# Performance work log

Measured on AMD Instinct MI355X. Metric: run time of the kernel, lower is better.

## Reference

```python
import jax, jax.numpy as jnp
import numpy as np
from jax import lax

HEADS, DHEAD, LMARK, PINV_ITERS = 8, 64, 256, 6
LN_EPS = 1e-5
DIM_IN, DIM_HID, N_CLASSES, N_INST = 1024, 512, 2, 16384


def layer_norm(x, g, b):
    mu = x.mean(-1, keepdims=True)
    var = ((x - mu) ** 2).mean(-1, keepdims=True)
    return (x - mu) * lax.rsqrt(var + LN_EPS) * g + b


def pinv_iter(x):
    # Newton-Schulz Moore-Penrose iteration (lucidrains nystrom-attention)
    ax = jnp.abs(x)
    z = jnp.swapaxes(x, -1, -2) / (ax.sum(-1).max() * ax.sum(-2).max())
    I = jnp.eye(x.shape[-1], dtype=x.dtype)
    for _ in range(PINV_ITERS):
        xz = x @ z
        z = 0.25 * z @ (13.0 * I - xz @ (15.0 * I - xz @ (7.0 * I - xz)))
    return z


def nystrom_attention(x, qkv_w, out_w, out_b, res_w):
    b, n, _ = x.shape
    pad = (-n) % LMARK  # pad at FRONT so n divisible by num_landmarks
    xp = jnp.pad(x, ((0, 0), (pad, 0), (0, 0)))
    npad = n + pad
    qkv = xp @ qkv_w.T  # (b, npad, 3*h*d)
    q, k, v = jnp.split(qkv, 3, axis=-1)
    sh = lambda t: t.reshape(b, npad, HEADS, DHEAD).transpose(0, 2, 1, 3)  # bhnd
    q, k, v = sh(q), sh(k), sh(v)
    q = q * (DHEAD ** -0.5)
    l = npad // LMARK  # tokens per landmark
    lm = lambda t: t.reshape(b, HEADS, LMARK, l, DHEAD).mean(3)
    ql, kl = lm(q), lm(k)
    a1 = jax.nn.softmax(jnp.einsum('bhid,bhjd->bhij', q, kl), -1)   # (b,h,npad,m)
    a2 = jax.nn.softmax(jnp.einsum('bhid,bhjd->bhij', ql, kl), -1)  # (b,h,m,m)
    a3 = jax.nn.softmax(jnp.einsum('bhid,bhjd->bhij', ql, k), -1)   # (b,h,m,npad)
    out = (a1 @ pinv_iter(a2)) @ (a3 @ v)
    # depthwise residual conv over sequence dim per head: kernel (33,1)
    res = lax.conv_general_dilated(v, res_w, (1, 1), [(16, 16), (0, 0)],
                                   dimension_numbers=('NCHW', 'OIHW', 'NCHW'),
                                   feature_group_count=HEADS)
    out = out + res
    out = out.transpose(0, 2, 1, 3).reshape(b, npad, HEADS * DHEAD)
    out = out @ out_w.T + out_b
    return out[:, -n:]


def depthwise(x, w, b, k):
    y = lax.conv_general_dilated(x, w, (1, 1), [(k // 2, k // 2)] * 2,
                                 dimension_numbers=('NCHW', 'OIHW', 'NCHW'),
                                 feature_group_count=x.shape[1])
    return y + b[None, :, None, None]


def ppeg(x, w7, b7, w5, b5, w3, b3):
    B, n1, C = x.shape
    cls_t, feat = x[:, :1], x[:, 1:]
    H = int(round(float(np.sqrt(n1 - 1))))
    f = feat.transpose(0, 2, 1).reshape(B, C, H, H)
    f = f + depthwise(f, w7, b7, 7) + depthwise(f, w5, b5, 5) + depthwise(f, w3, b3, 3)
    f = f.reshape(B, C, H * H).transpose(0, 2, 1)
    return jnp.concatenate([cls_t, f], axis=1)


def setup_inputs() -> dict:
    key = jax.random.key(0)
    ks = jax.random.split(key, 32)
    s = 0.02
    inner = HEADS * DHEAD
    d = {
        'X': jax.random.normal(ks[0], (1, N_INST, DIM_IN), jnp.float32),
        'fc1_w': jax.random.normal(ks[1], (DIM_HID, DIM_IN)) * s,
        'fc1_b': jnp.zeros((DIM_HID,)),
        'cls_token': jax.random.normal(ks[2], (1, 1, DIM_HID)),
        'ln1_g': jnp.ones((DIM_HID,)), 'ln1_b': jnp.zeros((DIM_HID,)),
        'qkv1_w': jax.random.normal(ks[3], (3 * inner, DIM_HID)) * s,
        'out1_w': jax.random.normal(ks[4], (DIM_HID, inner)) * s,
        'out1_b': jnp.zeros((DIM_HID,)),
        'res1_w': jax.random.normal(ks[5], (HEADS, 1, 33, 1)) * s,
        'w7': jax.random.normal(ks[6], (DIM_HID, 1, 7, 7)) * s, 'b7': jnp.zeros((DIM_HID,)),
        'w5': jax.random.normal(ks[7], (DIM_HID, 1, 5, 5)) * s, 'b5': jnp.zeros((DIM_HID,)),
        'w3': jax.random.normal(ks[8], (DIM_HID, 1, 3, 3)) * s, 'b3': jnp.zeros((DIM_HID,)),
        'ln2_g': jnp.ones((DIM_HID,)), 'ln2_b': jnp.zeros((DIM_HID,)),
        'qkv2_w': jax.random.normal(ks[9], (3 * inner, DIM_HID)) * s,
        'out2_w': jax.random.normal(ks[10], (DIM_HID, inner)) * s,
        'out2_b': jnp.zeros((DIM_HID,)),
        'res2_w': jax.random.normal(ks[11], (HEADS, 1, 33, 1)) * s,
        'lnf_g': jnp.ones((DIM_HID,)), 'lnf_b': jnp.zeros((DIM_HID,)),
        'fc2_w': jax.random.normal(ks[12], (N_CLASSES, DIM_HID)) * s,
        'fc2_b': jnp.zeros((N_CLASSES,)),
    }
    return d


def reference(X, fc1_w, fc1_b, cls_token, ln1_g, ln1_b, qkv1_w, out1_w, out1_b, res1_w,
              w7, b7, w5, b5, w3, b3, ln2_g, ln2_b, qkv2_w, out2_w, out2_b, res2_w,
              lnf_g, lnf_b, fc2_w, fc2_b):
    h = jax.nn.relu(X @ fc1_w.T + fc1_b)  # (1, N, dim_hid)
    B, Hn, C = h.shape
    _H = int(np.ceil(np.sqrt(Hn)))
    add_len = _H * _H - Hn
    h = jnp.concatenate([h, h[:, :add_len]], axis=1)  # pad to square by cycling
    h = jnp.concatenate([jnp.broadcast_to(cls_token, (B, 1, C)), h], axis=1)
    h = h + nystrom_attention(layer_norm(h, ln1_g, ln1_b), qkv1_w, out1_w, out1_b, res1_w)
    h = ppeg(h, w7, b7, w5, b5, w3, b3)
    h = h + nystrom_attention(layer_norm(h, ln2_g, ln2_b), qkv2_w, out2_w, out2_b, res2_w)
    h = layer_norm(h, lnf_g, lnf_b)[:, 0]
    return h @ fc2_w.T + fc2_b  # (1, n_classes)
```

## Files before the change

kernel.cpp:

```cpp
#include <hip/hip_runtime.h>
#include <hip/hip_bf16.h>

static const int S    = 16640;
static const int PADR = 255;
static const int NT   = 16385;
static const int CH   = 512;

typedef unsigned short u16;
typedef __attribute__((ext_vector_type(8))) short short8_t;
typedef __attribute__((ext_vector_type(4))) float float4_t;

__device__ __forceinline__ float b2f(u16 x) {
  union { unsigned u; float f; } t; t.u = (unsigned)x << 16; return t.f;
}
__device__ __forceinline__ u16 f2b(float x) {
  union { float f; unsigned u; } t; t.f = x;
  unsigned r = t.u + 0x7fff + ((t.u >> 16) & 1);
  return (u16)(r >> 16);
}

__device__ __forceinline__ float warpSum(float v) {
#pragma unroll
  for (int off = 32; off; off >>= 1) v += __shfl_xor(v, off);
  return v;
}
__device__ __forceinline__ float warpMax(float v) {
#pragma unroll
  for (int off = 32; off; off >>= 1) v = fmaxf(v, __shfl_xor(v, off));
  return v;
}
__device__ __forceinline__ float blockSum(float v) {
  __shared__ float sm[8];
  int lane = threadIdx.x & 63, wv = threadIdx.x >> 6;
  v = warpSum(v);
  __syncthreads();
  if (lane == 0) sm[wv] = v;
  __syncthreads();
  float t = 0.f;
  int nw = blockDim.x >> 6;
  for (int i = 0; i < nw; i++) t += sm[i];
  return t;
}
__device__ __forceinline__ float blockMax(float v) {
  __shared__ float sm[8];
  int lane = threadIdx.x & 63, wv = threadIdx.x >> 6;
  v = warpMax(v);
  __syncthreads();
  if (lane == 0) sm[wv] = v;
  __syncthreads();
  float t = -1e30f;
  int nw = blockDim.x >> 6;
  for (int i = 0; i < nw; i++) t = fmaxf(t, sm[i]);
  return t;
}

__global__ __launch_bounds__(256) void cvt_f2b(const float* __restrict__ in,
                                               u16* __restrict__ out, long n) {
  long i = ((long)blockIdx.x * 256 + threadIdx.x) * 4;
  if (i + 3 < n) {
    float4 v = *(const float4*)(in + i);
    out[i] = f2b(v.x); out[i + 1] = f2b(v.y); out[i + 2] = f2b(v.z); out[i + 3] = f2b(v.w);
  } else {
    for (long j = i; j < n; j++) out[j] = f2b(in[j]);
  }
}

__global__ __launch_bounds__(256) void wm_transpose(const float* __restrict__ Wm,
                                                    u16* __restrict__ WmT) {
  int n = blockIdx.x, head = blockIdx.y, k = threadIdx.x;
  WmT[((long)head * 64 + n) * 256 + k] = f2b(Wm[(long)head * 16384 + k * 64 + n]);
}

template <typename TA, int EPI>
__global__ __launch_bounds__(256) void mfma_gemm(
    const TA* __restrict__ A, const u16* __restrict__ B, float* __restrict__ C,
    const float* __restrict__ bias, int M, int N, int K,
    int lda, int ldb, int ldc,
    float alpha, float beta,
    u16* __restrict__ q_o, u16* __restrict__ k_o, u16* __restrict__ v_o, long s64)
{
  __shared__ u16 As[128][40];
  __shared__ u16 Bs[128][40];
  const int tid = threadIdx.x;
  const int m0 = blockIdx.y * 128, n0 = blockIdx.x * 128;
  const int wid = tid >> 6, lane = tid & 63;
  const int wr = wid >> 1, wc = wid & 1;
  const int l15 = lane & 15, l16 = lane >> 4;
  const int arow = tid >> 1, aseg = (tid & 1) * 16;
  float4_t acc[4][4] = {};

  for (int k0 = 0; k0 < K; k0 += 32) {
    {
      int gm = m0 + arow;
      u16 tmp[16];
      if (gm < M) {
        const TA* src = A + (long)gm * lda + k0 + aseg;
        if constexpr (sizeof(TA) == 2) {
          *(short8_t*)&tmp[0] = *(const short8_t*)src;
          *(short8_t*)&tmp[8] = *(const short8_t*)(src + 8);
        } else {
#pragma unroll
          for (int i4 = 0; i4 < 4; i4++) {
            float4 f = *(const float4*)((const float*)src + i4 * 4);
            tmp[i4 * 4 + 0] = f2b(f.x); tmp[i4 * 4 + 1] = f2b(f.y);
            tmp[i4 * 4 + 2] = f2b(f.z); tmp[i4 * 4 + 3] = f2b(f.w);
          }
        }
      } else {
#pragma unroll
        for (int i = 0; i < 16; i++) tmp[i] = 0;
      }
      *(short8_t*)&As[arow][aseg]     = *(short8_t*)&tmp[0];
      *(short8_t*)&As[arow][aseg + 8] = *(short8_t*)&tmp[8];
    }
    {
      int gn = n0 + arow;
      short8_t v0 = {}, v1 = {};
      if (gn < N) {
        const u16* src = B + (long)gn * ldb + k0 + aseg;
        v0 = *(const short8_t*)src; v1 = *(const short8_t*)(src + 8);
      }
      *(short8_t*)&Bs[arow][aseg]     = v0;
      *(short8_t*)&Bs[arow][aseg + 8] = v1;
    }
    __syncthreads();
    short8_t af[4], bfr[4];
#pragma unroll
    for (int i = 0; i < 4; i++)
      af[i] = *(const short8_t*)&As[wr * 64 + i * 16 + l15][l16 * 8];
#pragma unroll
    for (int i = 0; i < 4; i++)
      bfr[i] = *(const short8_t*)&Bs[wc * 64 + i * 16 + l15][l16 * 8];
#pragma unroll
    for (int i = 0; i < 4; i++)
#pragma unroll
      for (int j = 0; j < 4; j++)
        acc[i][j] = __builtin_amdgcn_mfma_f32_16x16x32_bf16(af[i], bfr[j], acc[i][j], 0, 0, 0);
    __syncthreads();
  }

#pragma unroll
  for (int mi = 0; mi < 4; mi++) {
#pragma unroll
    for (int ni = 0; ni < 4; ni++) {
#pragma unroll
      for (int j = 0; j < 4; j++) {
        int r = m0 + wr * 64 + mi * 16 + l16 * 4 + j;
        int c = n0 + wc * 64 + ni * 16 + l15;
        if (r >= M || c >= N) continue;
        float v = acc[mi][ni][j];
        if constexpr (EPI == 0) {
          long idx = (long)r * ldc + c;
          float o = alpha * v;
          if (bias) o += bias[c];
          if (beta != 0.f) o += beta * C[idx];
          C[idx] = o;
        } else if constexpr (EPI == 1) {
          long idx = (long)r * ldc + c;
          C[idx] = fmaxf(v + bias[c], 0.f);
        } else {
          int sec = c >> 9, hcol = c & 511;
          int head = hcol >> 6, d = hcol & 63;
          u16* dst = (sec == 0) ? q_o : (sec == 1 ? k_o : v_o);
          float o = (sec == 0) ? v * alpha : v;
          dst[(long)head * s64 + (long)r * 64 + d] = f2b(o);
        }
      }
    }
  }
}

template <int MODE>
__global__ __launch_bounds__(256) void pinv_gemm(
    const float* __restrict__ A, const float* __restrict__ B,
    float* __restrict__ C, float* __restrict__ C2, float alpha, float beta)
{
  __shared__ u16 Ah[32][40], Al[32][40], Bh[32][40], Bl[32][40];
  const int tid = threadIdx.x;
  const long zoff = (long)blockIdx.z << 16;
  A += zoff; B += zoff; C += zoff;
  if constexpr (MODE == 3) C2 += zoff;
  const int m0 = blockIdx.y * 32, n0 = blockIdx.x * 32;
  const int wid = tid >> 6, lane = tid & 63;
  const int wr = wid >> 1, wc = wid & 1;
  const int l15 = lane & 15, l16 = lane >> 4;
  const int arow = tid >> 3, acol = (tid & 7) * 4;
  float4_t acc = {};

  for (int k0 = 0; k0 < 256; k0 += 32) {
    {
      float4 va = *(const float4*)(A + (long)(m0 + arow) * 256 + k0 + acol);
      float4 vb = *(const float4*)(B + (long)(k0 + arow) * 256 + n0 + acol);
      float fa[4] = {va.x, va.y, va.z, va.w};
      float fb[4] = {vb.x, vb.y, vb.z, vb.w};
#pragma unroll
      for (int i = 0; i < 4; i++) {
        u16 hi = f2b(fa[i]);
        Ah[arow][acol + i] = hi;
        Al[arow][acol + i] = f2b(fa[i] - b2f(hi));
        u16 hj = f2b(fb[i]);
        Bh[acol + i][arow] = hj;
        Bl[acol + i][arow] = f2b(fb[i] - b2f(hj));
      }
    }
    __syncthreads();
    short8_t ah = *(const short8_t*)&Ah[wr * 16 + l15][l16 * 8];
    short8_t al = *(const short8_t*)&Al[wr * 16 + l15][l16 * 8];
    short8_t bh = *(const short8_t*)&Bh[wc * 16 + l15][l16 * 8];
    short8_t bl = *(const short8_t*)&Bl[wc * 16 + l15][l16 * 8];
    acc = __builtin_amdgcn_mfma_f32_16x16x32_bf16(ah, bh, acc, 0, 0, 0);
    acc = __builtin_amdgcn_mfma_f32_16x16x32_bf16(ah, bl, acc, 0, 0, 0);
    acc = __builtin_amdgcn_mfma_f32_16x16x32_bf16(al, bh, acc, 0, 0, 0);
    __syncthreads();
  }

#pragma unroll
  for (int j = 0; j < 4; j++) {
    int r = m0 + wr * 16 + l16 * 4 + j;
    int c = n0 + wc * 16 + l15;
    long idx = (long)r * 256 + c;
    float v = acc[j];
    if constexpr (MODE == 0) {
      C[idx] = alpha * v;
    } else if constexpr (MODE == 3) {
      C[idx] = v;
      C2[idx] = ((r == c) ? beta : 0.f) - v;
    } else {
      C[idx] = ((r == c) ? beta : 0.f) - v;
    }
  }
}

__global__ __launch_bounds__(256) void attn_a1(
    const u16* __restrict__ qb, const u16* __restrict__ klb,
    const u16* __restrict__ WmT, float* __restrict__ F, long s64)
{
  __shared__ u16 KW[256 * 72];
  __shared__ u16 Ps[64 * 136];
  const int tid = threadIdx.x;
  const int w = tid >> 6, lane = tid & 63;
  const int l15 = lane & 15, l16 = lane >> 4;
  const int head = blockIdx.y;
  const int row0 = blockIdx.x * 64 + w * 16;

  const u16* klh = klb + (long)head * 16384;
#pragma unroll
  for (int i = 0; i < 4; i++) {
    int idx = tid + i * 256;
    int row = idx >> 2, seg = (idx & 3) << 4;
    const u16* src = klh + row * 64 + seg;
    *(short8_t*)&KW[row * 72 + seg]     = *(const short8_t*)src;
    *(short8_t*)&KW[row * 72 + seg + 8] = *(const short8_t*)(src + 8);
  }
  short8_t aq[2];
#pragma unroll
  for (int slab = 0; slab < 2; slab++)
    aq[slab] = *(const short8_t*)(qb + (long)head * s64 + (long)(row0 + l15) * 64 + slab * 32 + l16 * 8);
  __syncthreads();

  float4_t sacc[16] = {};
#pragma unroll
  for (int nt = 0; nt < 16; nt++)
#pragma unroll
    for (int slab = 0; slab < 2; slab++) {
      short8_t bfr = *(const short8_t*)&KW[(nt * 16 + l15) * 72 + slab * 32 + l16 * 8];
      sacc[nt] = __builtin_amdgcn_mfma_f32_16x16x32_bf16(aq[slab], bfr, sacc[nt], 0, 0, 0);
    }
  float rcp[4];
#pragma unroll
  for (int reg = 0; reg < 4; reg++) {
    float m = -1e30f;
#pragma unroll
    for (int nt = 0; nt < 16; nt++) m = fmaxf(m, sacc[nt][reg]);
#pragma unroll
    for (int mk = 1; mk <= 8; mk <<= 1) m = fmaxf(m, __shfl_xor(m, mk));
    float s = 0.f;
#pragma unroll
    for (int nt = 0; nt < 16; nt++) { float e = __expf(sacc[nt][reg] - m); sacc[nt][reg] = e; s += e; }
#pragma unroll
    for (int mk = 1; mk <= 8; mk <<= 1) s += __shfl_xor(s, mk);
    rcp[reg] = 1.f / s;
  }
  __syncthreads();

  const u16* wmh = WmT + (long)head * 16384;
#pragma unroll
  for (int i = 0; i < 4; i++) {
    int idx = tid + i * 256;
    int row = idx >> 4, seg = (idx & 15) << 4;
    const u16* src = wmh + row * 256 + seg;
    *(short8_t*)&KW[row * 264 + seg]     = *(const short8_t*)src;
    *(short8_t*)&KW[row * 264 + seg + 8] = *(const short8_t*)(src + 8);
  }
#pragma unroll
  for (int nt = 0; nt < 8; nt++)
#pragma unroll
    for (int reg = 0; reg < 4; reg++)
      Ps[(w * 16 + 4 * l16 + reg) * 136 + nt * 16 + l15] = f2b(sacc[nt][reg]);
  __syncthreads();

  float4_t oacc[4] = {};
#pragma unroll
  for (int ks = 0; ks < 4; ks++) {
    short8_t pa = *(const short8_t*)&Ps[(w * 16 + l15) * 136 + ks * 32 + l16 * 8];
#pragma unroll
    for (int vt = 0; vt < 4; vt++) {
      short8_t bv = *(const short8_t*)&KW[(vt * 16 + l15) * 264 + ks * 32 + l16 * 8];
      oacc[vt] = __builtin_amdgcn_mfma_f32_16x16x32_bf16(pa, bv, oacc[vt], 0, 0, 0);
    }
  }
#pragma unroll
  for (int nt = 8; nt < 16; nt++)
#pragma unroll
    for (int reg = 0; reg < 4; reg++)
      Ps[(w * 16 + 4 * l16 + reg) * 136 + (nt - 8) * 16 + l15] = f2b(sacc[nt][reg]);
#pragma unroll
  for (int ks = 4; ks < 8; ks++) {
    short8_t pa = *(const short8_t*)&Ps[(w * 16 + l15) * 136 + (ks - 4) * 32 + l16 * 8];
#pragma unroll
    for (int vt = 0; vt < 4; vt++) {
      short8_t bv = *(const short8_t*)&KW[(vt * 16 + l15) * 264 + ks * 32 + l16 * 8];
      oacc[vt] = __builtin_amdgcn_mfma_f32_16x16x32_bf16(pa, bv, oacc[vt], 0, 0, 0);
    }
  }
#pragma unroll
  for (int vt = 0; vt < 4; vt++)
#pragma unroll
    for (int reg = 0; reg < 4; reg++) {
      int r = row0 + 4 * l16 + reg;
      F[(long)r * CH + head * 64 + vt * 16 + l15] = oacc[vt][reg] * rcp[reg];
    }
}

__global__ __launch_bounds__(256) void attn_a3v_split(
    const u16* __restrict__ qlb, const u16* __restrict__ kb,
    const u16* __restrict__ vb,
    float* __restrict__ pm, float* __restrict__ pl, float* __restrict__ poacc,
    long s64)
{
  __shared__ u16 Vt[64][136];
  __shared__ u16 Kt[128 * 72];
  __shared__ u16 Ps[4][16][136];
  const int tid = threadIdx.x;
  const int w = tid >> 6, lane = tid & 63;
  const int l15 = lane & 15, l16 = lane >> 4;
  const int head = blockIdx.y;
  const int split = blockIdx.z;
  const int row0 = blockIdx.x * 64 + w * 16;

  short8_t aq[2];
#pragma unroll
  for (int slab = 0; slab < 2; slab++)
    aq[slab] = *(const short8_t*)(qlb + (long)head * 16384 + (long)(row0 + l15) * 64 + slab * 32 + l16 * 8);

  float m[4], l[4];
  float4_t oacc[4] = {};
#pragma unroll
  for (int r = 0; r < 4; r++) { m[r] = -1e30f; l[r] = 0.f; }

  const u16* kh = kb + (long)head * s64;
  const u16* vh = vb + (long)head * s64;
  const int vrow = tid >> 1, vhalf = (tid & 1) * 32;

  const int kt0 = split * 10;
  for (int kt = kt0; kt < kt0 + 10; kt++) {
    const int j0 = kt * 128;
    __syncthreads();
    {
      const u16* src = vh + (long)(j0 + vrow) * 64 + vhalf;
#pragma unroll
      for (int i = 0; i < 32; i++) Vt[vhalf + i][vrow] = src[i];
    }
#pragma unroll
    for (int i = 0; i < 2; i++) {
      int idx = tid + i * 256;
      int row = idx >> 2, seg = (idx & 3) << 4;
      const u16* src = kh + (long)(j0 + row) * 64 + seg;
      *(short8_t*)&Kt[row * 72 + seg]     = *(const short8_t*)src;
      *(short8_t*)&Kt[row * 72 + seg + 8] = *(const short8_t*)(src + 8);
    }
    __syncthreads();
    float4_t sacc[8] = {};
#pragma unroll
    for (int nt = 0; nt < 8; nt++)
#pragma unroll
      for (int slab = 0; slab < 2; slab++) {
        short8_t bfr = *(const short8_t*)&Kt[(nt * 16 + l15) * 72 + slab * 32 + l16 * 8];
        sacc[nt] = __builtin_amdgcn_mfma_f32_16x16x32_bf16(aq[slab], bfr, sacc[nt], 0, 0, 0);
      }
    float scale[4];
#pragma unroll
    for (int reg = 0; reg < 4; reg++) {
      float tm = -1e30f;
#pragma unroll
      for (int nt = 0; nt < 8; nt++) tm = fmaxf(tm, sacc[nt][reg]);
#pragma unroll
      for (int mk = 1; mk <= 8; mk <<= 1) tm = fmaxf(tm, __shfl_xor(tm, mk));
      float nm = fmaxf(m[reg], tm);
      scale[reg] = __expf(m[reg] - nm);
      m[reg] = nm;
      float ts = 0.f;
#pragma unroll
      for (int nt = 0; nt < 8; nt++) {
        float e = __expf(sacc[nt][reg] - nm);
        sacc[nt][reg] = e; ts += e;
      }
#pragma unroll
      for (int mk = 1; mk <= 8; mk <<= 1) ts += __shfl_xor(ts, mk);
      l[reg] = l[reg] * scale[reg] + ts;
#pragma unroll
      for (int vt = 0; vt < 4; vt++) oacc[vt][reg] *= scale[reg];
    }
#pragma unroll
    for (int nt = 0; nt < 8; nt++)
#pragma unroll
      for (int reg = 0; reg < 4; reg++)
        Ps[w][4 * l16 + reg][nt * 16 + l15] = f2b(sacc[nt][reg]);
#pragma unroll
    for (int ks = 0; ks < 4; ks++) {
      short8_t pa = *(const short8_t*)&Ps[w][l15][ks * 32 + l16 * 8];
#pragma unroll
      for (int vt = 0; vt < 4; vt++) {
        short8_t bv = *(const short8_t*)&Vt[vt * 16 + l15][ks * 32 + l16 * 8];
        oacc[vt] = __builtin_amdgcn_mfma_f32_16x16x32_bf16(pa, bv, oacc[vt], 0, 0, 0);
      }
    }
  }
#pragma unroll
  for (int reg = 0; reg < 4; reg++) {
    int r = row0 + 4 * l16 + reg;
    long pidx = ((long)(head * 13 + split) << 8) + r;
    if (l15 == 0) { pm[pidx] = m[reg]; pl[pidx] = l[reg]; }
#pragma unroll
    for (int vt = 0; vt < 4; vt++)
      poacc[(pidx << 6) + vt * 16 + l15] = oacc[vt][reg];
  }
}

__global__ __launch_bounds__(64) void a3v_merge(const float* __restrict__ pm,
    const float* __restrict__ pl, const float* __restrict__ poacc,
    float* __restrict__ w3v)
{
  int hb = blockIdx.x;
  int head = hb >> 8, row = hb & 255;
  int d = threadIdx.x;
  float M = -1e30f;
  for (int sp = 0; sp < 13; sp++)
    M = fmaxf(M, pm[((long)(head * 13 + sp) << 8) + row]);
  float num = 0.f, den = 0.f;
  for (int sp = 0; sp < 13; sp++) {
    long pidx = ((long)(head * 13 + sp) << 8) + row;
    float sc = __expf(pm[pidx] - M);
    den += pl[pidx] * sc;
    num += poacc[(pidx << 6) + d] * sc;
  }
  w3v[((long)head << 14) + ((long)row << 6) + d] = num / den;
}

template <bool BT, int MODE>
__global__ __launch_bounds__(256) void mm_kernel(
    const float* __restrict__ A, const float* __restrict__ Bm, float* __restrict__ C,
    const float* __restrict__ bias,
    int M, int N, int K, int lda, int ldb, int ldc,
    long sA, long sB, long sC, float alpha, float beta, long s64)
{
  __shared__ float As[16][64];
  __shared__ float Bs[16][64];
  const int bz = blockIdx.z;
  A  += (long)bz * sA;
  Bm += (long)bz * sB;
  C  += (long)bz * sC;
  const int m0 = blockIdx.y * 64, n0 = blockIdx.x * 64;
  const int tid = threadIdx.x;
  const int tm = tid >> 4, tn = tid & 15;
  const int ar = tid >> 2;
  const int ac = (tid & 3) << 2;
  float acc[4][4] = {};
  for (int k0 = 0; k0 < K; k0 += 16) {
#pragma unroll
    for (int i = 0; i < 4; i++) {
      int gm = m0 + ar, gk = k0 + ac + i;
      As[ac + i][ar] = (gm < M && gk < K) ? A[(long)gm * lda + gk] : 0.f;
    }
    if constexpr (BT) {
#pragma unroll
      for (int i = 0; i < 4; i++) {
        int gn = n0 + ar, gk = k0 + ac + i;
        Bs[ac + i][ar] = (gn < N && gk < K) ? Bm[(long)gn * ldb + gk] : 0.f;
      }
    } else {
      int bk = tid >> 4;
      int bn = (tid & 15) << 2;
#pragma unroll
      for (int i = 0; i < 4; i++) {
        int gk = k0 + bk, gn = n0 + bn + i;
        Bs[bk][bn + i] = (gk < K && gn < N) ? Bm[(long)gk * ldb + gn] : 0.f;
      }
    }
    __syncthreads();
#pragma unroll
    for (int kk = 0; kk < 16; kk++) {
      float a[4], b[4];
#pragma unroll
      for (int i = 0; i < 4; i++) { a[i] = As[kk][tm * 4 + i]; b[i] = Bs[kk][tn * 4 + i]; }
#pragma unroll
      for (int i = 0; i < 4; i++)
#pragma unroll
        for (int j = 0; j < 4; j++)
          acc[i][j] = fmaf(a[i], b[j], acc[i][j]);
    }
    __syncthreads();
  }
#pragma unroll
  for (int i = 0; i < 4; i++) {
    int row = m0 + tm * 4 + i;
    if (row >= M) continue;
#pragma unroll
    for (int j = 0; j < 4; j++) {
      int col = n0 + tn * 4 + j;
      if (col >= N) continue;
      long idx = (long)row * ldc + col;
      float v = acc[i][j];
      float o = alpha * v;
      if (bias) o += bias[col];
      C[idx] = (beta != 0.f) ? o + beta * C[idx] : o;
    }
  }
}

__global__ void cls_copy(const float* __restrict__ c, float* __restrict__ h) {
  h[threadIdx.x] = c[threadIdx.x];
}

__global__ __launch_bounds__(256) void ln_pad_b(const float* __restrict__ h,
    const float* __restrict__ g, const float* __restrict__ b,
    u16* __restrict__ out, int pad)
{
  int s = blockIdx.x, t = threadIdx.x;
  u16* o = out + (long)s * CH;
  if (s < pad) { o[t] = 0; o[t + 256] = 0; return; }
  const float* x = h + (long)(s - pad) * CH;
  float x0 = x[t], x1 = x[t + 256];
  float mu = blockSum(x0 + x1) * (1.f / 512.f);
  float d0 = x0 - mu, d1 = x1 - mu;
  float var = blockSum(d0 * d0 + d1 * d1) * (1.f / 512.f);
  float rs = rsqrtf(var + 1e-5f);
  o[t]       = f2b(d0 * rs * g[t]       + b[t]);
  o[t + 256] = f2b(d1 * rs * g[t + 256] + b[t + 256]);
}

__global__ __launch_bounds__(64) void landmark_b(const u16* __restrict__ q,
    float* __restrict__ ql, u16* __restrict__ qlb) {
  int hb = blockIdx.x;
  int d = threadIdx.x;
  int hh = hb >> 8, j = hb & 255;
  const u16* src = q + ((long)hh * S + (long)j * 65) * 64 + d;
  float s = 0.f;
  for (int g2 = 0; g2 < 65; g2++) s += b2f(src[(long)g2 * 64]);
  s *= (1.f / 65.f);
  ql[(long)hb * 64 + d] = s;
  qlb[(long)hb * 64 + d] = f2b(s);
}

__global__ __launch_bounds__(256) void rowsoftmax(float* __restrict__ X) {
  float* row = X + (long)blockIdx.x * 256;
  int t = threadIdx.x;
  float x = row[t];
  float m = blockMax(x);
  float e = __expf(x - m);
  float s = blockSum(e);
  row[t] = e / s;
}

__global__ __launch_bounds__(256) void colabs(const float* __restrict__ a2, float* __restrict__ cs) {
  int hb = blockIdx.x; int hh = hb >> 8, j = hb & 255;
  float s = blockSum(fabsf(a2[((long)hh * 256 + threadIdx.x) * 256 + j]));
  if (threadIdx.x == 0) cs[hb] = s;
}
__global__ __launch_bounds__(256) void scaleinv(const float* __restrict__ cs,
                                                float* __restrict__ inv) {
  float m2 = -1e30f;
  for (int i = threadIdx.x; i < 2048; i += 256) m2 = fmaxf(m2, cs[i]);
  m2 = blockMax(m2);
  if (threadIdx.x == 0) inv[0] = 1.f / m2;
}
__global__ __launch_bounds__(256) void z0k(const float* __restrict__ a2,
                                           const float* __restrict__ inv, float* __restrict__ z) {
  int hb = blockIdx.x; int hh = hb >> 8, i = hb & 255; int j = threadIdx.x;
  z[(long)hb * 256 + j] = a2[((long)hh * 256 + j) * 256 + i] * inv[0];
}

__global__ __launch_bounds__(256) void resconv2(const u16* __restrict__ v,
    const float* __restrict__ w, float* __restrict__ F)
{
  __shared__ u16 T[160][64];
  __shared__ float ws[33];
  const int hh = blockIdx.y;
  const int p0 = blockIdx.x * 128;
  const int tid = threadIdx.x;
  if (tid < 33) ws[tid] = w[hh * 33 + tid];
  const u16* vh = v + (long)hh * S * 64;
  for (int idx = tid; idx < 640; idx += 256) {
    int row = idx >> 2, seg = (idx & 3) * 16;
    int j = p0 - 16 + row;
    short8_t a = {}, b = {};
    if (0 <= j && j < S) {
      const u16* src = vh + (long)j * 64 + seg;
      a = *(const short8_t*)src; b = *(const short8_t*)(src + 8);
    }
    *(short8_t*)&T[row][seg]     = a;
    *(short8_t*)&T[row][seg + 8] = b;
  }
  __syncthreads();
  const int d = tid & 63;
  const int pg = tid >> 6;
  float wreg[33];
#pragma unroll
  for (int t = 0; t < 33; t++) wreg[t] = ws[t];
#pragma unroll
  for (int g = 0; g < 4; g++) {
    const int base = pg * 32 + g * 8;
    float win[40];
#pragma unroll
    for (int i = 0; i < 40; i++) win[i] = b2f(T[base + i][d]);
#pragma unroll
    for (int p = 0; p < 8; p++) {
      float acc = 0.f;
#pragma unroll
      for (int t = 0; t < 33; t++) acc = fmaf(wreg[t], win[p + t], acc);
      F[(long)(p0 + base + p) * CH + hh * 64 + d] += acc;
    }
  }
}

__global__ __launch_bounds__(256) void transpose_feat(const float* __restrict__ h, float* __restrict__ f) {
  __shared__ float tile[32][33];
  int p0 = blockIdx.x * 32;
  int c0 = blockIdx.y * 32;
  int tx = threadIdx.x & 31, ty = threadIdx.x >> 5;
  for (int i = 0; i < 32; i += 8)
    tile[ty + i][tx] = h[(long)(1 + p0 + ty + i) * CH + c0 + tx];
  __syncthreads();
  for (int i = 0; i < 32; i += 8)
    f[(long)(c0 + ty + i) * 16384 + p0 + tx] = tile[tx][ty + i];
}

__global__ __launch_bounds__(256) void ppeg_tile(const float* __restrict__ f,
    const float* __restrict__ w7, const float* __restrict__ b7,
    const float* __restrict__ w5, const float* __restrict__ b5,
    const float* __restrict__ w3, const float* __restrict__ b3,
    float* __restrict__ fo)
{
  __shared__ float T[38][40];
  __shared__ float W7s[49], W5s[25], W3s[9];
  int c = blockIdx.y;
  int ty0 = (blockIdx.x >> 2) * 32, tx0 = (blockIdx.x & 3) * 32;
  int tid = threadIdx.x;
  if (tid < 49) W7s[tid] = w7[c * 49 + tid];
  if (tid < 25) W5s[tid] = w5[c * 25 + tid];
  if (tid < 9)  W3s[tid] = w3[c * 9 + tid];
  const float* fc = f + (long)c * 16384;
  for (int idx = tid; idx < 38 * 38; idx += 256) {
    int r = idx / 38, cc = idx - r * 38;
    int y = ty0 + r - 3, x = tx0 + cc - 3;
    T[r][cc] = (0 <= y && y < 128 && 0 <= x && x < 128) ? fc[y * 128 + x] : 0.f;
  }
  __syncthreads();
  float bsum = b7[c] + b5[c] + b3[c];
#pragma unroll
  for (int p = 0; p < 4; p++) {
    int px = tid + p * 256;
    int y = px >> 5, x = px & 31;
    float acc = T[y + 3][x + 3] + bsum;
#pragma unroll
    for (int dy = 0; dy < 7; dy++)
#pragma unroll
      for (int dx = 0; dx < 7; dx++)
        acc += W7s[dy * 7 + dx] * T[y + dy][x + dx];
#pragma unroll
    for (int dy = 0; dy < 5; dy++)
#pragma unroll
      for (int dx = 0; dx < 5; dx++)
        acc += W5s[dy * 5 + dx] * T[y + dy + 1][x + dx + 1];
#pragma unroll
    for (int dy = 0; dy < 3; dy++)
#pragma unroll
      for (int dx = 0; dx < 3; dx++)
        acc += W3s[dy * 3 + dx] * T[y + dy + 2][x + dx + 2];
    fo[(long)c * 16384 + (ty0 + y) * 128 + tx0 + x] = acc;
  }
}

__global__ __launch_bounds__(256) void transpose_back(const float* __restrict__ fo, float* __restrict__ h) {
  __shared__ float tile[32][33];
  int p0 = blockIdx.x * 32;
  int c0 = blockIdx.y * 32;
  int tx = threadIdx.x & 31, ty = threadIdx.x >> 5;
  for (int i = 0; i < 32; i += 8)
    tile[ty + i][tx] = fo[(long)(c0 + ty + i) * 16384 + p0 + tx];
  __syncthreads();
  for (int i = 0; i < 32; i += 8)
    h[(long)(1 + p0 + ty + i) * CH + c0 + tx] = tile[tx][ty + i];
}

__global__ __launch_bounds__(256) void final_k(const float* __restrict__ h,
    const float* __restrict__ g, const float* __restrict__ b,
    const float* __restrict__ w, const float* __restrict__ fb, float* __restrict__ out)
{
  int t = threadIdx.x;
  float x0 = h[t], x1 = h[t + 256];
  float mu = blockSum(x0 + x1) * (1.f / 512.f);
  float d0 = x0 - mu, d1 = x1 - mu;
  float var = blockSum(d0 * d0 + d1 * d1) * (1.f / 512.f);
  float rs = rsqrtf(var + 1e-5f);
  float y0 = d0 * rs * g[t]       + b[t];
  float y1 = d1 * rs * g[t + 256] + b[t + 256];
  float s0 = blockSum(y0 * w[t]       + y1 * w[t + 256]);
  float s1 = blockSum(y0 * w[512 + t] + y1 * w[512 + t + 256]);
  if (t == 0) {
    out[0] = s0 + fb[0];
    out[1] = s1 + fb[1];
  }
}

struct AttnW {
  const float *lng, *lnb, *qkvw, *outw, *outb, *resw;
};

static void run_attn(const AttnW& Wt, const u16* qkvw_b, const u16* outw_b,
                     float* h, u16* hn_b, u16* qb, u16* kb, u16* vb, float* F,
                     float* ql, float* kl, u16* qlb, u16* klb,
                     float* w3v, float* Wm, u16* WmT_b,
                     float* a2, float* xz, float* t1, float* t2, float* zA, float* zB,
                     float* cs, float* inv,
                     float* pm, float* pl, float* poacc,
                     hipStream_t stream)
{
  const long s64 = (long)S * 64;
  ln_pad_b<<<S, 256, 0, stream>>>(h, Wt.lng, Wt.lnb, hn_b, PADR);
  mfma_gemm<u16, 2><<<dim3(12, 130, 1), 256, 0, stream>>>(
      hn_b, qkvw_b, nullptr, nullptr, S, 1536, 512, 512, 512, 0,
      0.125f, 0.f, qb, kb, vb, s64);
  landmark_b<<<2048, 64, 0, stream>>>(qb, ql, qlb);
  landmark_b<<<2048, 64, 0, stream>>>(kb, kl, klb);
  mm_kernel<true, 0><<<dim3(4, 4, 8), 256, 0, stream>>>(
      ql, kl, a2, nullptr, 256, 256, 64, 64, 64, 256, 16384, 16384, 65536, 1.f, 0.f, 0);
  rowsoftmax<<<2048, 256, 0, stream>>>(a2);
  colabs<<<2048, 256, 0, stream>>>(a2, cs);
  scaleinv<<<1, 256, 0, stream>>>(cs, inv);
  z0k<<<2048, 256, 0, stream>>>(a2, inv, zA);
  float* zc = zA; float* zo = zB;
  for (int it = 0; it < 6; it++) {
    pinv_gemm<3><<<dim3(8, 8, 8), 256, 0, stream>>>(a2, zc, xz, t1, 1.f, 7.f);
    pinv_gemm<4><<<dim3(8, 8, 8), 256, 0, stream>>>(xz, t1, t2, nullptr, 1.f, 15.f);
    pinv_gemm<4><<<dim3(8, 8, 8), 256, 0, stream>>>(xz, t2, t1, nullptr, 1.f, 13.f);
    pinv_gemm<0><<<dim3(8, 8, 8), 256, 0, stream>>>(zc, t1, zo, nullptr, 0.25f, 0.f);
    float* tmp = zc; zc = zo; zo = tmp;
  }
  attn_a3v_split<<<dim3(4, 8, 13), 256, 0, stream>>>(qlb, kb, vb, pm, pl, poacc, s64);
  a3v_merge<<<2048, 64, 0, stream>>>(pm, pl, poacc, w3v);
  mm_kernel<false, 0><<<dim3(1, 4, 8), 256, 0, stream>>>(
      zc, w3v, Wm, nullptr, 256, 64, 256, 256, 64, 64, 65536, 16384, 16384, 1.f, 0.f, 0);
  wm_transpose<<<dim3(64, 8, 1), 256, 0, stream>>>(Wm, WmT_b);
  attn_a1<<<dim3(260, 8, 1), 256, 0, stream>>>(qb, klb, WmT_b, F, s64);
  resconv2<<<dim3(130, 8, 1), 256, 0, stream>>>(vb, Wt.resw, F);
  mfma_gemm<float, 0><<<dim3(4, 129, 1), 256, 0, stream>>>(
      F + (long)PADR * CH, outw_b, h, Wt.outb, NT, 512, 512, 512, 512, 512,
      1.f, 1.f, nullptr, nullptr, nullptr, 0);
}

extern "C" void kernel_launch(void* const* d_in, const int* in_sizes, int n_in,
                              void* d_out, int out_size, void* d_ws, size_t ws_size,
                              hipStream_t stream)
{
  const float* X      = (const float*)d_in[0];
  const float* fc1w   = (const float*)d_in[1];
  const float* fc1b   = (const float*)d_in[2];
  const float* clstok = (const float*)d_in[3];
  AttnW w1{ (const float*)d_in[4], (const float*)d_in[5], (const float*)d_in[6],
            (const float*)d_in[7], (const float*)d_in[8], (const float*)d_in[9] };
  const float* w7 = (const float*)d_in[10]; const float* b7 = (const float*)d_in[11];
  const float* w5 = (const float*)d_in[12]; const float* b5 = (const float*)d_in[13];
  const float* w3 = (const float*)d_in[14]; const float* b3 = (const float*)d_in[15];
  AttnW w2{ (const float*)d_in[16], (const float*)d_in[17], (const float*)d_in[18],
            (const float*)d_in[19], (const float*)d_in[20], (const float*)d_in[21] };
  const float* lnfg = (const float*)d_in[22];
  const float* lnfb = (const float*)d_in[23];
  const float* fc2w = (const float*)d_in[24];
  const float* fc2b = (const float*)d_in[25];
  float* out = (float*)d_out;

  char* wsb = (char*)d_ws;
  size_t off = 0;
  auto alloc = [&](size_t nbytes) {
    void* p = wsb + off;
    off = (off + nbytes + 255) & ~(size_t)255;
    return p;
  };
  float* h    = (float*)alloc((size_t)NT * CH * 4);
  float* F    = (float*)alloc((size_t)S * CH * 4);
  u16*  hn_b  = (u16*)alloc((size_t)S * CH * 2);
  u16*  qb    = (u16*)alloc((size_t)S * CH * 2);
  u16*  kb    = (u16*)alloc((size_t)S * CH * 2);
  u16*  vb    = (u16*)alloc((size_t)S * CH * 2);
  char* big   = (char*)alloc(33554432);
  u16*  fc1w_b = (u16*)alloc(524288 * 2);
  u16*  qkv1_b = (u16*)alloc(786432 * 2);
  u16*  qkv2_b = (u16*)alloc(786432 * 2);
  u16*  out1_b = (u16*)alloc(262144 * 2);
  u16*  out2_b = (u16*)alloc(262144 * 2);
  float* ql   = (float*)alloc(131072 * 4);
  float* kl   = (float*)alloc(131072 * 4);
  u16*  qlb   = (u16*)alloc(131072 * 2);
  u16*  klb   = (u16*)alloc(131072 * 2);
  float* w3v  = (float*)alloc(131072 * 4);
  float* Wm   = (float*)alloc(131072 * 4);
  u16*  WmT_b = (u16*)alloc(131072 * 2);
  float* a2   = (float*)alloc(524288 * 4);
  float* xz   = (float*)alloc(524288 * 4);
  float* t1   = (float*)alloc(524288 * 4);
  float* t2   = (float*)alloc(524288 * 4);
  float* zA   = (float*)alloc(524288 * 4);
  float* zB   = (float*)alloc(524288 * 4);
  float* cs   = (float*)alloc(2048 * 4);
  float* inv  = (float*)alloc(256);
  float* pm   = (float*)alloc((size_t)8 * 13 * 256 * 4);
  float* pl   = (float*)alloc((size_t)8 * 13 * 256 * 4);
  float* poacc = (float*)alloc((size_t)8 * 13 * 256 * 64 * 4);
  (void)in_sizes; (void)n_in; (void)out_size; (void)ws_size;

  cvt_f2b<<<512, 256, 0, stream>>>(fc1w, fc1w_b, 524288);
  cvt_f2b<<<768, 256, 0, stream>>>(w1.qkvw, qkv1_b, 786432);
  cvt_f2b<<<768, 256, 0, stream>>>(w2.qkvw, qkv2_b, 786432);
  cvt_f2b<<<256, 256, 0, stream>>>(w1.outw, out1_b, 262144);
  cvt_f2b<<<256, 256, 0, stream>>>(w2.outw, out2_b, 262144);

  cls_copy<<<1, 512, 0, stream>>>(clstok, h);
  mfma_gemm<float, 1><<<dim3(4, 128, 1), 256, 0, stream>>>(
      X, fc1w_b, h + CH, fc1b, 16384, 512, 1024, 1024, 1024, 512,
      1.f, 0.f, nullptr, nullptr, nullptr, 0);

  run_attn(w1, qkv1_b, out1_b, h, hn_b, qb, kb, vb, F, ql, kl, qlb, klb,
           w3v, Wm, WmT_b, a2, xz, t1, t2, zA, zB, cs, inv,
           pm, pl, poacc, stream);

  float* fppeg = (float*)big;
  transpose_feat<<<dim3(512, 16, 1), 256, 0, stream>>>(h, fppeg);
  ppeg_tile<<<dim3(16, 512, 1), 256, 0, stream>>>(fppeg, w7, b7, w5, b5, w3, b3, F);
  transpose_back<<<dim3(512, 16, 1), 256, 0, stream>>>(F, h);

  run_attn(w2, qkv2_b, out2_b, h, hn_b, qb, kb, vb, F, ql, kl, qlb, klb,
           w3v, Wm, WmT_b, a2, xz, t1, t2, zA, zB, cs, inv,
           pm, pl, poacc, stream);

  final_k<<<1, 256, 0, stream>>>(h, lnfg, lnfb, fc2w, fc2b, out);
}
```

Measured before the change: 1.218 ms.

## Fuse pinv iterations into one cooperative kernel, remap GEMM tiles per XCD, merge landmark launches

The 24 small pinv GEMM launches become a single cooperative kernel that uses grid-wide syncs between steps, removing per-launch overhead and gaps. The tiled MFMA GEMM remaps its block index so that consecutive tiles stay on the same XCD, which is meant to improve L2 locality. The two landmark-mean launches are merged into one. Grid syncs add their own cost, and the cooperative launch needs all 512 blocks to be resident at once.

```diff
diff --git a/kernel.cpp b/kernel.cpp
--- a/kernel.cpp
+++ b/kernel.cpp
@@ -1,5 +1,8 @@
 #include <hip/hip_runtime.h>
 #include <hip/hip_bf16.h>
+#include <hip/hip_cooperative_groups.h>
+
+namespace cg = cooperative_groups;
 
 static const int S    = 16640;
 static const int PADR = 255;
@@ -82,7 +85,14 @@
   __shared__ u16 As[128][40];
   __shared__ u16 Bs[128][40];
   const int tid = threadIdx.x;
-  const int m0 = blockIdx.y * 128, n0 = blockIdx.x * 128;
+  const int nwg = gridDim.x * gridDim.y;
+  int lid = blockIdx.y * gridDim.x + blockIdx.x;
+  {
+    const int qq = nwg >> 3, rr = nwg & 7;
+    const int xcd = lid & 7, loc = lid >> 3;
+    lid = (xcd < rr ? xcd * (qq + 1) : rr * (qq + 1) + (xcd - rr) * qq) + loc;
+  }
+  const int m0 = (lid / gridDim.x) * 128, n0 = (lid % gridDim.x) * 128;
   const int wid = tid >> 6, lane = tid & 63;
   const int wr = wid >> 1, wc = wid & 1;
   const int l15 = lane & 15, l16 = lane >> 4;
@@ -171,16 +181,17 @@
 }
 
 template <int MODE>
-__global__ __launch_bounds__(256) void pinv_gemm(
+__device__ __forceinline__ void pinv_step(
     const float* __restrict__ A, const float* __restrict__ B,
-    float* __restrict__ C, float* __restrict__ C2, float alpha, float beta)
-{
-  __shared__ u16 Ah[32][40], Al[32][40], Bh[32][40], Bl[32][40];
+    float* __restrict__ C, float* __restrict__ C2, float alpha, float beta,
+    u16 (*Ah)[40], u16 (*Al)[40], u16 (*Bh)[40], u16 (*Bl)[40])
+{
   const int tid = threadIdx.x;
-  const long zoff = (long)blockIdx.z << 16;
+  const int flat = blockIdx.x;
+  const long zoff = (long)(flat >> 6) << 16;
+  const int m0 = ((flat >> 3) & 7) * 32, n0 = (flat & 7) * 32;
   A += zoff; B += zoff; C += zoff;
   if constexpr (MODE == 3) C2 += zoff;
-  const int m0 = blockIdx.y * 32, n0 = blockIdx.x * 32;
   const int wid = tid >> 6, lane = tid & 63;
   const int wr = wid >> 1, wc = wid & 1;
   const int l15 = lane & 15, l16 = lane >> 4;
@@ -228,6 +239,22 @@
     } else {
       C[idx] = ((r == c) ? beta : 0.f) - v;
     }
+  }
+}
+
+__global__ __launch_bounds__(256, 2) void pinv_chain(
+    const float* __restrict__ a2, float* __restrict__ zA, float* __restrict__ zB,
+    float* __restrict__ xz, float* __restrict__ t1, float* __restrict__ t2)
+{
+  __shared__ u16 Ah[32][40], Al[32][40], Bh[32][40], Bl[32][40];
+  cg::grid_group grid = cg::this_grid();
+  float* zc = zA; float* zo = zB;
+  for (int it = 0; it < 6; it++) {
+    pinv_step<3>(a2, zc, xz, t1, 1.f, 7.f, Ah, Al, Bh, Bl);      grid.sync();
+    pinv_step<4>(xz, t1, t2, nullptr, 1.f, 15.f, Ah, Al, Bh, Bl); grid.sync();
+    pinv_step<4>(xz, t2, t1, nullptr, 1.f, 13.f, Ah, Al, Bh, Bl); grid.sync();
+    pinv_step<0>(zc, t1, zo, nullptr, 0.25f, 0.f, Ah, Al, Bh, Bl); grid.sync();
+    float* t = zc; zc = zo; zo = t;
   }
 }
 
@@ -549,17 +576,23 @@
   o[t + 256] = f2b(d1 * rs * g[t + 256] + b[t + 256]);
 }
 
-__global__ __launch_bounds__(64) void landmark_b(const u16* __restrict__ q,
-    float* __restrict__ ql, u16* __restrict__ qlb) {
-  int hb = blockIdx.x;
+__global__ __launch_bounds__(64) void landmark_b2(const u16* __restrict__ q,
+    const u16* __restrict__ k,
+    float* __restrict__ ql, float* __restrict__ kl,
+    u16* __restrict__ qlb, u16* __restrict__ klb) {
+  int isK = blockIdx.x >> 11;
+  int hb = blockIdx.x & 2047;
   int d = threadIdx.x;
   int hh = hb >> 8, j = hb & 255;
-  const u16* src = q + ((long)hh * S + (long)j * 65) * 64 + d;
+  const u16* base = isK ? k : q;
+  const u16* src = base + ((long)hh * S + (long)j * 65) * 64 + d;
   float s = 0.f;
   for (int g2 = 0; g2 < 65; g2++) s += b2f(src[(long)g2 * 64]);
   s *= (1.f / 65.f);
-  ql[(long)hb * 64 + d] = s;
-  qlb[(long)hb * 64 + d] = f2b(s);
+  float* outf = isK ? kl : ql;
+  u16* outb = isK ? klb : qlb;
+  outf[(long)hb * 64 + d] = s;
+  outb[(long)hb * 64 + d] = f2b(s);
 }
 
 __global__ __launch_bounds__(256) void rowsoftmax(float* __restrict__ X) {
@@ -741,26 +774,24 @@
   mfma_gemm<u16, 2><<<dim3(12, 130, 1), 256, 0, stream>>>(
       hn_b, qkvw_b, nullptr, nullptr, S, 1536, 512, 512, 512, 0,
       0.125f, 0.f, qb, kb, vb, s64);
-  landmark_b<<<2048, 64, 0, stream>>>(qb, ql, qlb);
-  landmark_b<<<2048, 64, 0, stream>>>(kb, kl, klb);
+  landmark_b2<<<4096, 64, 0, stream>>>(qb, kb, ql, kl, qlb, klb);
   mm_kernel<true, 0><<<dim3(4, 4, 8), 256, 0, stream>>>(
       ql, kl, a2, nullptr, 256, 256, 64, 64, 64, 256, 16384, 16384, 65536, 1.f, 0.f, 0);
   rowsoftmax<<<2048, 256, 0, stream>>>(a2);
   colabs<<<2048, 256, 0, stream>>>(a2, cs);
   scaleinv<<<1, 256, 0, stream>>>(cs, inv);
   z0k<<<2048, 256, 0, stream>>>(a2, inv, zA);
-  float* zc = zA; float* zo = zB;
-  for (int it = 0; it < 6; it++) {
-    pinv_gemm<3><<<dim3(8, 8, 8), 256, 0, stream>>>(a2, zc, xz, t1, 1.f, 7.f);
-    pinv_gemm<4><<<dim3(8, 8, 8), 256, 0, stream>>>(xz, t1, t2, nullptr, 1.f, 15.f);
-    pinv_gemm<4><<<dim3(8, 8, 8), 256, 0, stream>>>(xz, t2, t1, nullptr, 1.f, 13.f);
-    pinv_gemm<0><<<dim3(8, 8, 8), 256, 0, stream>>>(zc, t1, zo, nullptr, 0.25f, 0.f);
-    float* tmp = zc; zc = zo; zo = tmp;
+  {
+    const float* a2c = a2;
+    void* args[6] = { (void*)&a2c, (void*)&zA, (void*)&zB,
+                      (void*)&xz, (void*)&t1, (void*)&t2 };
+    hipLaunchCooperativeKernel((const void*)pinv_chain, dim3(512), dim3(256),
+                               args, 0, stream);
   }
   attn_a3v_split<<<dim3(4, 8, 13), 256, 0, stream>>>(qlb, kb, vb, pm, pl, poacc, s64);
   a3v_merge<<<2048, 64, 0, stream>>>(pm, pl, poacc, w3v);
   mm_kernel<false, 0><<<dim3(1, 4, 8), 256, 0, stream>>>(
-      zc, w3v, Wm, nullptr, 256, 64, 256, 256, 64, 64, 65536, 16384, 16384, 1.f, 0.f, 0);
+      zA, w3v, Wm, nullptr, 256, 64, 256, 256, 64, 64, 65536, 16384, 16384, 1.f, 0.f, 0);
   wm_transpose<<<dim3(64, 8, 1), 256, 0, stream>>>(Wm, WmT_b);
   attn_a1<<<dim3(260, 8, 1), 256, 0, stream>>>(qb, klb, WmT_b, F, s64);
   resconv2<<<dim3(130, 8, 1), 256, 0, stream>>>(vb, Wt.resw, F);
```

After: 4.075 ms. +234.5%, slower.
